# Optimization experiments

Measured on AMD Instinct MI355X. Metric: run time of the kernel, lower is better.

## Reference

```python
import jax, jax.numpy as jnp
import numpy as np

SIZE = 64
B, NMAX = 8, 24


def setup_inputs() -> dict:
    key = jax.random.key(0)
    ks = jax.random.split(key, 8)
    # valid boxes: top-left in [0,400), width/height in [10,210)
    xy = jax.random.uniform(ks[0], (B, NMAX, 2)) * 400.0
    wh = jax.random.uniform(ks[1], (B, NMAX, 2)) * 200.0 + 10.0
    bboxes = jnp.concatenate([xy, xy + wh], axis=-1)  # [B,N,4] (x1,y1,x2,y2)
    num_obj = jax.random.randint(ks[2], (B,), 2, NMAX + 1)
    conv1_w = jax.random.normal(ks[3], (64, 2, 5, 5)) * 0.1
    conv1_b = jnp.zeros((64,), jnp.float32)
    conv2_w = jax.random.normal(ks[4], (32, 64, 5, 5)) * 0.05
    conv2_b = jnp.zeros((32,), jnp.float32)
    lin_w = jax.random.normal(ks[5], (5408, 4800)) * 0.01
    lin_b = jnp.zeros((4800,), jnp.float32)
    return dict(bboxes=bboxes, num_obj=num_obj, conv1_w=conv1_w, conv1_b=conv1_b,
                conv2_w=conv2_w, conv2_b=conv2_b, lin_w=lin_w, lin_b=lin_b)


def _pair_indices(num_obj):
    # ragged pair construction on host; num_obj is an integer constant input
    n = np.asarray(num_obj)
    bs, is_, js = [], [], []
    for b in range(n.shape[0]):
        ii, jj = np.triu_indices(int(n[b]), k=1)
        bs.append(np.full(ii.shape, b, dtype=np.int32))
        is_.append(ii.astype(np.int32))
        js.append(jj.astype(np.int32))
    return np.concatenate(bs), np.concatenate(is_), np.concatenate(js)


def _get_sp(boxA, boxB):
    # DRG-style spatial map: rescale both boxes into the union-box frame
    # (aspect preserving, shorter axis centered), rasterize as binary masks.
    # boxA, boxB: [M,4] -> [M,2,64,64]
    u1 = jnp.minimum(boxA[:, 0], boxB[:, 0])
    v1 = jnp.minimum(boxA[:, 1], boxB[:, 1])
    u2 = jnp.maximum(boxA[:, 2], boxB[:, 2])
    v2 = jnp.maximum(boxA[:, 3], boxB[:, 3])
    w = u2 - u1
    h = v2 - v1
    scale = (SIZE - 1.0) / jnp.maximum(jnp.maximum(w, h), 1e-6)
    offx = jnp.where(h >= w, (SIZE - 1.0 - w * scale) * 0.5, 0.0)
    offy = jnp.where(w > h, (SIZE - 1.0 - h * scale) * 0.5, 0.0)

    xs = jnp.arange(SIZE, dtype=jnp.float32)[None, None, :]
    ys = jnp.arange(SIZE, dtype=jnp.float32)[None, :, None]

    def rast(box):
        x1 = jnp.round((box[:, 0] - u1) * scale + offx)[:, None, None]
        y1 = jnp.round((box[:, 1] - v1) * scale + offy)[:, None, None]
        x2 = jnp.round((box[:, 2] - u1) * scale + offx)[:, None, None]
        y2 = jnp.round((box[:, 3] - v1) * scale + offy)[:, None, None]
        m = (xs >= x1) & (xs <= x2) & (ys >= y1) & (ys <= y2)
        return m.astype(jnp.float32)

    return jnp.stack([rast(boxA), rast(boxB)], axis=1)


def _conv(x, w, b):
    y = jax.lax.conv_general_dilated(x, w, (1, 1), 'VALID',
                                     dimension_numbers=('NCHW', 'OIHW', 'NCHW'))
    return y + b[None, :, None, None]


def _pool(x):
    return jax.lax.reduce_window(x, -jnp.inf, jax.lax.max,
                                 (1, 1, 2, 2), (1, 1, 2, 2), 'VALID')


def reference(bboxes, num_obj, conv1_w, conv1_b, conv2_w, conv2_b, lin_w, lin_b):
    bi, ii, ji = _pair_indices(num_obj)
    boxA = bboxes[bi, ii]                       # [M,4]
    boxB = bboxes[bi, ji]                       # [M,4]
    sp = _get_sp(boxA, boxB)                    # [M,2,64,64]
    x = jax.nn.relu(_conv(sp, conv1_w, conv1_b))   # [M,64,60,60]
    x = _pool(x)                                   # [M,64,30,30]
    x = jax.nn.relu(_conv(x, conv2_w, conv2_b))    # [M,32,26,26]
    x = _pool(x)                                   # [M,32,13,13]
    x = x.reshape(x.shape[0], -1)                  # [M,5408]
    feat = jax.nn.relu(x @ lin_w + lin_b)          # [M,4800]
    slicing = jnp.stack([jnp.asarray(bi), jnp.asarray(ii), jnp.asarray(ji)],
                        axis=1).astype(jnp.float32)  # [M,3]
    return feat, slicing
```

## Files before the change

### kernel.cpp

```cpp
#include <hip/hip_runtime.h>
#include <hip/hip_bf16.h>

typedef __attribute__((ext_vector_type(8))) short short8;
typedef __attribute__((ext_vector_type(4))) float f32x4;

__device__ inline unsigned short f2bf(float x) {
  unsigned u = __float_as_uint(x);
  unsigned rounding = 0x7FFFu + ((u >> 16) & 1u);
  return (unsigned short)((u + rounding) >> 16);
}
__device__ inline float bf2f(unsigned short u) {
  return __uint_as_float(((unsigned)u) << 16);
}
__device__ inline void gload_lds16(const void* g, void* l) {
  __builtin_amdgcn_global_load_lds(
      (const __attribute__((address_space(1))) unsigned int*)g,
      (__attribute__((address_space(3))) unsigned int*)l, 16, 0, 0);
}

#define KPAD 5440
#define NPAD 4864
#define X1Q  32768

__global__ void prep_pairs(const float* __restrict__ bboxes,
                           const int* __restrict__ num_obj, int M,
                           int* __restrict__ pairTab,
                           float* __restrict__ slicing) {
  __shared__ int cum[9];
  if (threadIdx.x == 0) {
    int c = 0; cum[0] = 0;
    for (int b = 0; b < 8; b++) { int n = num_obj[b]; c += n*(n-1)/2; cum[b+1] = c; }
  }
  __syncthreads();
  for (int m = threadIdx.x; m < M; m += blockDim.x) {
    int b = 0;
    while (b < 7 && m >= cum[b+1]) b++;
    int p = m - cum[b];
    int n = num_obj[b];
    int i = 0, rem = p;
    while (rem >= (n - 1 - i)) { rem -= (n - 1 - i); i++; }
    int j = i + 1 + rem;
    const float* A = bboxes + (b*24 + i)*4;
    const float* Bb = bboxes + (b*24 + j)*4;
    float ax1=A[0], ay1=A[1], ax2=A[2], ay2=A[3];
    float bx1=Bb[0], by1=Bb[1], bx2=Bb[2], by2=Bb[3];
    float u1 = fminf(ax1,bx1), v1 = fminf(ay1,by1);
    float u2 = fmaxf(ax2,bx2), v2 = fmaxf(ay2,by2);
    float w = u2-u1, h = v2-v1;
    float scale = 63.0f / fmaxf(fmaxf(w,h), 1e-6f);
    float offx = (h >= w) ? __fmul_rn(63.0f - __fmul_rn(w,scale), 0.5f) : 0.0f;
    float offy = (w > h)  ? __fmul_rn(63.0f - __fmul_rn(h,scale), 0.5f) : 0.0f;
    int* t = pairTab + m*8;
    t[0] = (int)rintf(__fadd_rn(__fmul_rn(ax1-u1, scale), offx));
    t[1] = (int)rintf(__fadd_rn(__fmul_rn(ay1-v1, scale), offy));
    t[2] = (int)rintf(__fadd_rn(__fmul_rn(ax2-u1, scale), offx));
    t[3] = (int)rintf(__fadd_rn(__fmul_rn(ay2-v1, scale), offy));
    t[4] = (int)rintf(__fadd_rn(__fmul_rn(bx1-u1, scale), offx));
    t[5] = (int)rintf(__fadd_rn(__fmul_rn(by1-v1, scale), offy));
    t[6] = (int)rintf(__fadd_rn(__fmul_rn(bx2-u1, scale), offx));
    t[7] = (int)rintf(__fadd_rn(__fmul_rn(by2-v1, scale), offy));
    slicing[m*3+0] = (float)b;
    slicing[m*3+1] = (float)i;
    slicing[m*3+2] = (float)j;
  }
}

__global__ void prep_tables(const float* __restrict__ w1, const float* __restrict__ b1,
                            const float* __restrict__ w2,
                            float* __restrict__ T, unsigned short* __restrict__ W2B) {
  int idx = blockIdx.x*256 + threadIdx.x;
  if (idx < 86528) {
    int o = idx & 63;
    int t = idx >> 6;
    int rxi = t % 26; t /= 26;
    int ryi = t % 26;
    int c = t / 26;
    int ky0 = ryi/5, ky1 = ryi%5, kx0 = rxi/5, kx1 = rxi%5;
    float s = 0.f;
    for (int ky = ky0; ky <= ky1; ky++)
      for (int kx = kx0; kx <= kx1; kx++)
        s += w1[((o*2 + c)*5 + ky)*5 + kx];
    T[idx] = s + 0.5f * b1[o];
  } else if (idx < 86528 + 53248) {
    int i = idx - 86528;
    int j = i & 7;
    int ln = (i >> 3) & 63;
    int r1 = i >> 9;
    int mt = r1 & 1;
    int r2 = r1 >> 1;
    int s = r2 % 13;
    int pp = r2 / 13;
    int oc = mt*16 + (ln & 15);
    int q = ln >> 4;
    int kyx = 2*s + (q >> 1);
    int ic = pp*16 + ((q & 1) << 3) + j;
    float val = 0.f;
    if (kyx < 25) val = w2[((oc*64 + ic)*5 + kyx/5)*5 + (kyx%5)];
    W2B[i] = f2bf(val);
  }
}

__global__ __launch_bounds__(256) void prep_wt(const float* __restrict__ lw,
                                               unsigned short* __restrict__ Wt) {
  __shared__ unsigned short tile[64][65];
  int k0 = blockIdx.x*64, n0 = blockIdx.y*64;
  for (int i = threadIdx.x; i < 64*64; i += 256) {
    int r = i >> 6, cdx = i & 63;
    int k = k0 + r, n = n0 + cdx;
    float v = (k < 5408) ? lw[(size_t)k*4800 + n] : 0.f;
    tile[r][cdx] = f2bf(v);
  }
  __syncthreads();
  for (int i = threadIdx.x; i < 64*64; i += 256) {
    int r = i >> 6, cdx = i & 63;
    int n = n0 + r, k = k0 + cdx;
    Wt[(size_t)n*KPAD + k] = tile[cdx][r];
  }
}

__global__ __launch_bounds__(256) void conv1_pool(
    const int* __restrict__ pairTab, const float* __restrict__ T,
    unsigned short* __restrict__ X1) {
  __shared__ unsigned char rIdx[4][64];
  int blk = blockIdx.x;
  int m = blk >> 2, pp = blk & 3;
  int tid = threadIdx.x;
  const int* pt = pairTab + m*8;

  if (tid < 240) {
    int qq = tid % 60, which = tid / 60;
    int lo, hi;
    if (which == 0)      { lo = pt[1]; hi = pt[3]; }
    else if (which == 1) { lo = pt[5]; hi = pt[7]; }
    else if (which == 2) { lo = pt[0]; hi = pt[2]; }
    else                 { lo = pt[4]; hi = pt[6]; }
    int k0 = lo - qq; if (k0 < 0) k0 = 0;
    int k1 = hi - qq; if (k1 > 4) k1 = 4;
    rIdx[which][qq] = (k0 > k1) ? (unsigned char)25 : (unsigned char)(k0*5 + k1);
  }
  __syncthreads();

  char* X1q = (char*)X1 + (size_t)blk * X1Q;
  for (int item = tid; item < 1800; item += 256) {
    int pos = item >> 1;
    int icg = item & 1;
    int ch0 = pp*16 + icg*8;
    int py = pos / 30, px = pos % 30;
    float best[8];
#pragma unroll
    for (int j = 0; j < 8; j++) best[j] = -1e30f;
#pragma unroll
    for (int d = 0; d < 4; d++) {
      int y = py*2 + (d>>1), x = px*2 + (d&1);
      int rya = rIdx[0][y], ryb = rIdx[1][y];
      int rxa = rIdx[2][x], rxb = rIdx[3][x];
      const float* Ta = T + (((rya)*26 + rxa)<<6) + ch0;
      const float* Tb = T + (((26 + ryb)*26 + rxb)<<6) + ch0;
      f32x4 a0 = *(const f32x4*)Ta, a1 = *(const f32x4*)(Ta+4);
      f32x4 c0 = *(const f32x4*)Tb, c1 = *(const f32x4*)(Tb+4);
#pragma unroll
      for (int j = 0; j < 4; j++) {
        best[j]   = fmaxf(best[j],   a0[j]+c0[j]);
        best[4+j] = fmaxf(best[4+j], a1[j]+c1[j]);
      }
    }
    short8 v;
#pragma unroll
    for (int j = 0; j < 8; j++)
      v[j] = (short)f2bf(fmaxf(best[j], 0.f));
    int byte = pos*32 + ((icg ^ ((pos>>2)&1))<<4);
    *(short8*)(X1q + byte) = v;
  }
}

__global__ __launch_bounds__(512) void conv2_mfma(
    const unsigned short* __restrict__ X1, const unsigned short* __restrict__ W2B,
    const float* __restrict__ b2, unsigned short* __restrict__ X, int M) {
  __shared__ char smem[2*X1Q];
  int m = blockIdx.x;
  int tid = threadIdx.x, lane = tid & 63, wid = tid >> 6;
  const char* X1m = (const char*)X1 + (size_t)m*4*X1Q;

  int ntile = (wid < 4) ? 6 : 5;
  int tstart = (wid < 4) ? wid*6 : 24 + (wid-4)*5;
  int rowbase[6];
#pragma unroll
  for (int tt = 0; tt < 6; tt++) {
    int pos = (tstart + tt)*16 + (lane & 15);
    if (pos > 675) pos = 675;
    rowbase[tt] = (pos/26)*30 + (pos % 26);
  }
  f32x4 acc[6][2];
#pragma unroll
  for (int tt = 0; tt < 6; tt++) {
    acc[tt][0] = (f32x4){0.f,0.f,0.f,0.f};
    acc[tt][1] = (f32x4){0.f,0.f,0.f,0.f};
  }

  int q = lane >> 4;
  int qh = q >> 1;
  int qs = q & 1;

  auto stageq = [&](int buf, int qtr) {
    const char* src = X1m + (size_t)qtr * X1Q;
    char* dst = smem + buf * X1Q;
#pragma unroll
    for (int c = 0; c < 4; c++) {
      int chunk = wid + c*8;
      gload_lds16(src + chunk*1024 + lane*16, dst + chunk*1024);
    }
  };

  stageq(0, 0);
  __syncthreads();
  for (int pp = 0; pp < 4; pp++) {
    if (pp < 3) stageq((pp+1) & 1, pp+1);
    const char* pb = smem + (pp & 1) * X1Q;
    for (int s = 0; s < 13; s++) {
      const unsigned short* wptr = W2B + (size_t)(pp*13 + s)*1024 + lane*8;
      short8 a0 = *(const short8*)wptr;
      short8 a1 = *(const short8*)(wptr + 512);
      int kyx = 2*s + qh; if (kyx > 24) kyx = 24;
      int radd = (kyx/5)*30 + (kyx%5);
#pragma unroll
      for (int tt = 0; tt < 6; tt++) {
        if (tt < ntile) {
          int row = rowbase[tt] + radd;
          int byte = row*32 + ((qs ^ ((row>>2)&1))<<4);
          short8 bv = *(const short8*)(pb + byte);
          acc[tt][0] = __builtin_amdgcn_mfma_f32_16x16x32_bf16(a0, bv, acc[tt][0], 0, 0, 0);
          acc[tt][1] = __builtin_amdgcn_mfma_f32_16x16x32_bf16(a1, bv, acc[tt][1], 0, 0, 0);
        }
      }
    }
    __syncthreads();
  }
  unsigned short* p1 = (unsigned short*)smem;
#pragma unroll
  for (int tt = 0; tt < 6; tt++) {
    if (tt < ntile) {
      int pos = (tstart + tt)*16 + (lane & 15);
      if (pos <= 675) {
#pragma unroll
        for (int mt = 0; mt < 2; mt++)
#pragma unroll
          for (int r = 0; r < 4; r++) {
            int oc = mt*16 + q*4 + r;
            p1[oc*676 + pos] = f2bf(acc[tt][mt][r]);
          }
      }
    }
  }
  __syncthreads();
  for (int f = tid; f < 5408; f += 512) {
    int oc = f / 169, rem = f % 169;
    int py = rem / 13, px = rem % 13;
    const unsigned short* c2 = p1 + oc*676 + py*52 + px*2;
    float v = fmaxf(fmaxf(bf2f(c2[0]), bf2f(c2[1])), fmaxf(bf2f(c2[26]), bf2f(c2[27])));
    X[(size_t)m*KPAD + f] = f2bf(fmaxf(v + b2[oc], 0.f));
  }
  if (tid < 32) X[(size_t)m*KPAD + 5408 + tid] = 0;
}

__global__ __launch_bounds__(256) void gemm_lin(
    const unsigned short* __restrict__ X, const unsigned short* __restrict__ Wt,
    const float* __restrict__ lin_b, float* __restrict__ P, float* __restrict__ out,
    int M, int Mpad, int splits) {
  __shared__ unsigned short As[2][4096];
  __shared__ unsigned short Bs[2][8192];
  int tid = threadIdx.x, lane = tid & 63, wid = tid >> 6;
  int m0 = blockIdx.x * 64, n0 = blockIdx.y * 128;
  int ks = blockIdx.z;
  int itBeg = (ks * 85) / splits, itEnd = ((ks + 1) * 85) / splits;
  int wm = wid >> 1, wn = wid & 1;

  f32x4 acc[2][4];
#pragma unroll
  for (int i = 0; i < 2; i++)
#pragma unroll
    for (int j = 0; j < 4; j++) acc[i][j] = (f32x4){0.f,0.f,0.f,0.f};

  int rsub = lane >> 3;
  int kslot = (lane & 7) ^ rsub;
  int kg = lane >> 4;

  auto stage = [&](int buf, int it) {
    size_t kof = (size_t)it * 64 + kslot * 8;
#pragma unroll
    for (int cc = 0; cc < 2; cc++) {
      int chunk = wid + cc*4;
      int gm = m0 + chunk*8 + rsub;
      gload_lds16(X + (size_t)gm*KPAD + kof, (char*)As[buf] + chunk*1024);
    }
#pragma unroll
    for (int cc = 0; cc < 4; cc++) {
      int chunk = wid + cc*4;
      int gn = n0 + chunk*8 + rsub;
      gload_lds16(Wt + (size_t)gn*KPAD + kof, (char*)Bs[buf] + chunk*1024);
    }
  };

  stage(0, itBeg);
  __syncthreads();
  int cur = 0;
  for (int it = itBeg; it < itEnd; ++it) {
    if (it + 1 < itEnd) stage(cur ^ 1, it + 1);
#pragma unroll
    for (int ksub = 0; ksub < 2; ++ksub) {
      int slot = ksub*4 + kg;
      short8 af[2], bfr[4];
#pragma unroll
      for (int mf = 0; mf < 2; mf++) {
        int r = wm*32 + mf*16 + (lane & 15);
        af[mf] = *(const short8*)((const char*)As[cur] + r*128 + ((slot ^ (lane&7))<<4));
      }
#pragma unroll
      for (int nf = 0; nf < 4; nf++) {
        int r = wn*64 + nf*16 + (lane & 15);
        bfr[nf] = *(const short8*)((const char*)Bs[cur] + r*128 + ((slot ^ (lane&7))<<4));
      }
#pragma unroll
      for (int mf = 0; mf < 2; mf++)
#pragma unroll
        for (int nf = 0; nf < 4; nf++)
          acc[mf][nf] = __builtin_amdgcn_mfma_f32_16x16x32_bf16(af[mf], bfr[nf], acc[mf][nf], 0, 0, 0);
    }
    __syncthreads();
    cur ^= 1;
  }

  if (splits == 1) {
#pragma unroll
    for (int mf = 0; mf < 2; mf++)
#pragma unroll
      for (int nf = 0; nf < 4; nf++) {
        int n = n0 + wn*64 + nf*16 + (lane & 15);
#pragma unroll
        for (int r = 0; r < 4; r++) {
          int mm = m0 + wm*32 + mf*16 + ((lane>>4)<<2) + r;
          if (mm < M && n < 4800)
            out[(size_t)mm*4800 + n] = fmaxf(acc[mf][nf][r] + lin_b[n], 0.f);
        }
      }
  } else {
    float* Pp = P + (size_t)ks * Mpad * NPAD;
#pragma unroll
    for (int mf = 0; mf < 2; mf++)
#pragma unroll
      for (int nf = 0; nf < 4; nf++) {
        int n = n0 + wn*64 + nf*16 + (lane & 15);
#pragma unroll
        for (int r = 0; r < 4; r++) {
          int mm = m0 + wm*32 + mf*16 + ((lane>>4)<<2) + r;
          Pp[(size_t)mm*NPAD + n] = acc[mf][nf][r];
        }
      }
  }
}

__global__ void reduce_out(const float* __restrict__ P, const float* __restrict__ lb,
                           float* __restrict__ out, int M, int Mpad, int splits) {
  int total = M * 1200;
  for (int idx = blockIdx.x*256 + threadIdx.x; idx < total; idx += gridDim.x*256) {
    int m = idx / 1200, qq = idx - m*1200;
    int n = qq * 4;
    f32x4 s = *(const f32x4*)(P + (size_t)m*NPAD + n);
    for (int sidx = 1; sidx < splits; sidx++)
      s += *(const f32x4*)(P + (size_t)sidx*Mpad*NPAD + (size_t)m*NPAD + n);
    f32x4 b = *(const f32x4*)(lb + n);
    f32x4 r;
#pragma unroll
    for (int j = 0; j < 4; j++) r[j] = fmaxf(s[j] + b[j], 0.f);
    *(f32x4*)(out + (size_t)m*4800 + n) = r;
  }
}

extern "C" void kernel_launch(void* const* d_in, const int* in_sizes, int n_in,
                              void* d_out, int out_size, void* d_ws, size_t ws_size,
                              hipStream_t stream) {
  const float* bboxes = (const float*)d_in[0];
  const int*   num_obj = (const int*)d_in[1];
  const float* w1 = (const float*)d_in[2];
  const float* b1 = (const float*)d_in[3];
  const float* w2 = (const float*)d_in[4];
  const float* b2 = (const float*)d_in[5];
  const float* lw = (const float*)d_in[6];
  const float* lb = (const float*)d_in[7];
  float* out = (float*)d_out;
  int M = out_size / 4803;
  int Mpad = (M + 63) & ~63;

  auto align512 = [](size_t x) { return (x + 511) & ~(size_t)511; };
  size_t fixed = 0;
  fixed += align512((size_t)M*8*4);
  fixed += align512((size_t)86528*4);
  fixed += align512((size_t)53248*2);
  fixed += align512((size_t)4800*KPAD*2);
  fixed += align512((size_t)Mpad*KPAD*2);
  fixed += align512((size_t)M*4*X1Q);
  int splits = 4;
  while (splits > 1 && fixed + align512((size_t)splits*Mpad*NPAD*4) > ws_size) splits >>= 1;

  char* ws = (char*)d_ws;
  size_t off = 0;
  auto alloc = [&](size_t bytes) {
    off = align512(off);
    char* p = ws + off;
    off += bytes;
    return p;
  };
  int* pairTab = (int*)alloc((size_t)M*8*4);
  float* T = (float*)alloc((size_t)86528*4);
  unsigned short* W2B = (unsigned short*)alloc((size_t)53248*2);
  unsigned short* Wt = (unsigned short*)alloc((size_t)4800*KPAD*2);
  unsigned short* X = (unsigned short*)alloc((size_t)Mpad*KPAD*2);
  unsigned short* X1 = (unsigned short*)alloc((size_t)M*4*X1Q);
  float* P = (splits > 1) ? (float*)alloc((size_t)splits*Mpad*NPAD*4) : nullptr;

  prep_pairs<<<1, 256, 0, stream>>>(bboxes, num_obj, M, pairTab, out + (size_t)M*4800);
  prep_tables<<<(86528+53248+255)/256, 256, 0, stream>>>(w1, b1, w2, T, W2B);
  prep_wt<<<dim3(85, 75), 256, 0, stream>>>(lw, Wt);
  conv1_pool<<<M*4, 256, 0, stream>>>(pairTab, T, X1);
  conv2_mfma<<<M, 512, 0, stream>>>(X1, W2B, b2, X, M);
  gemm_lin<<<dim3(Mpad/64, 38, splits), 256, 0, stream>>>(X, Wt, lb, P, out, M, Mpad, splits);
  if (splits > 1)
    reduce_out<<<1024, 256, 0, stream>>>(P, lb, out, M, Mpad, splits);
}
```

Baseline: 346.5 us.

## Split conv2 per pair into two row-halves with smaller blocks and LDS

The conv2 MFMA kernel now launches two 256-thread blocks per pair instead of one 512-thread block. Each block computes half of the output rows: rows 0-13 for the first block and rows 14-25 for the second. It stages only the input rows that half needs, into a smaller double-buffered LDS region. The goal is more blocks, less LDS per block and higher occupancy, so more pairs' conv2 work can overlap. The cost is some redundant input loading across the halo rows and more per-wave tiles per block.

```diff
diff --git a/kernel.cpp b/kernel.cpp
--- a/kernel.cpp
+++ b/kernel.cpp
@@ -21,6 +21,7 @@
 #define KPAD 5440
 #define NPAD 4864
 #define X1Q  32768
+#define SBUF 17408
 
 __global__ void prep_pairs(const float* __restrict__ bboxes,
                            const int* __restrict__ num_obj, int M,
@@ -173,22 +174,32 @@
   }
 }
 
-__global__ __launch_bounds__(512) void conv2_mfma(
+__global__ __launch_bounds__(256) void conv2_mfma(
     const unsigned short* __restrict__ X1, const unsigned short* __restrict__ W2B,
     const float* __restrict__ b2, unsigned short* __restrict__ X, int M) {
-  __shared__ char smem[2*X1Q];
-  int m = blockIdx.x;
+  __shared__ char smem[2*SBUF];
+  int blk = blockIdx.x;
+  int m = blk >> 1, h = blk & 1;
   int tid = threadIdx.x, lane = tid & 63, wid = tid >> 6;
   const char* X1m = (const char*)X1 + (size_t)m*4*X1Q;
 
-  int ntile = (wid < 4) ? 6 : 5;
-  int tstart = (wid < 4) ? wid*6 : 24 + (wid-4)*5;
+  int oy0    = h ? 14 : 0;
+  int npos   = h ? 312 : 364;
+  int ntiles = h ? 20 : 23;
+  int row0   = h ? 416 : 0;
+  int ncall  = h ? 16 : 17;
+
+  int tbase = ntiles >> 2, trem = ntiles & 3;
+  int ntile  = tbase + (wid < trem ? 1 : 0);
+  int tstart = (wid < trem) ? wid*(tbase+1) : trem*(tbase+1) + (wid-trem)*tbase;
+
   int rowbase[6];
 #pragma unroll
   for (int tt = 0; tt < 6; tt++) {
     int pos = (tstart + tt)*16 + (lane & 15);
-    if (pos > 675) pos = 675;
-    rowbase[tt] = (pos/26)*30 + (pos % 26);
+    if (pos > npos-1) pos = npos-1;
+    int oy = oy0 + pos/26;
+    rowbase[tt] = oy*30 + pos%26;
   }
   f32x4 acc[6][2];
 #pragma unroll
@@ -197,17 +208,16 @@
     acc[tt][1] = (f32x4){0.f,0.f,0.f,0.f};
   }
 
-  int q = lane >> 4;
-  int qh = q >> 1;
-  int qs = q & 1;
+  int q = lane >> 4, qh = q >> 1, qs = q & 1;
 
   auto stageq = [&](int buf, int qtr) {
-    const char* src = X1m + (size_t)qtr * X1Q;
-    char* dst = smem + buf * X1Q;
-#pragma unroll
-    for (int c = 0; c < 4; c++) {
-      int chunk = wid + c*8;
-      gload_lds16(src + chunk*1024 + lane*16, dst + chunk*1024);
+    const char* src = X1m + (size_t)qtr * X1Q + row0*32;
+    char* dst = smem + buf * SBUF;
+#pragma unroll
+    for (int c = 0; c < 5; c++) {
+      int chunk = wid + c*4;
+      if (chunk < ncall)
+        gload_lds16(src + chunk*1024 + lane*16, dst + chunk*1024);
     }
   };
 
@@ -215,7 +225,7 @@
   __syncthreads();
   for (int pp = 0; pp < 4; pp++) {
     if (pp < 3) stageq((pp+1) & 1, pp+1);
-    const char* pb = smem + (pp & 1) * X1Q;
+    const char* pb = smem + (pp & 1) * SBUF;
     for (int s = 0; s < 13; s++) {
       const unsigned short* wptr = W2B + (size_t)(pp*13 + s)*1024 + lane*8;
       short8 a0 = *(const short8*)wptr;
@@ -226,7 +236,7 @@
       for (int tt = 0; tt < 6; tt++) {
         if (tt < ntile) {
           int row = rowbase[tt] + radd;
-          int byte = row*32 + ((qs ^ ((row>>2)&1))<<4);
+          int byte = (row - row0)*32 + ((qs ^ ((row>>2)&1))<<4);
           short8 bv = *(const short8*)(pb + byte);
           acc[tt][0] = __builtin_amdgcn_mfma_f32_16x16x32_bf16(a0, bv, acc[tt][0], 0, 0, 0);
           acc[tt][1] = __builtin_amdgcn_mfma_f32_16x16x32_bf16(a1, bv, acc[tt][1], 0, 0, 0);
@@ -240,26 +250,30 @@
   for (int tt = 0; tt < 6; tt++) {
     if (tt < ntile) {
       int pos = (tstart + tt)*16 + (lane & 15);
-      if (pos <= 675) {
+      if (pos < npos) {
 #pragma unroll
         for (int mt = 0; mt < 2; mt++)
 #pragma unroll
           for (int r = 0; r < 4; r++) {
             int oc = mt*16 + q*4 + r;
-            p1[oc*676 + pos] = f2bf(acc[tt][mt][r]);
+            p1[oc*npos + pos] = f2bf(acc[tt][mt][r]);
           }
       }
     }
   }
   __syncthreads();
-  for (int f = tid; f < 5408; f += 512) {
-    int oc = f / 169, rem = f % 169;
-    int py = rem / 13, px = rem % 13;
-    const unsigned short* c2 = p1 + oc*676 + py*52 + px*2;
+  int nout = h ? 6 : 7;
+  int oypb = h ? 7 : 0;
+  for (int f = tid; f < 32*nout*13; f += 256) {
+    int ocl = f / (nout*13), rem2 = f % (nout*13);
+    int oyl = rem2 / 13, px = rem2 % 13;
+    int oyp = oypb + oyl;
+    int posl = (oyp*2 - oy0)*26 + px*2;
+    const unsigned short* c2 = p1 + ocl*npos + posl;
     float v = fmaxf(fmaxf(bf2f(c2[0]), bf2f(c2[1])), fmaxf(bf2f(c2[26]), bf2f(c2[27])));
-    X[(size_t)m*KPAD + f] = f2bf(fmaxf(v + b2[oc], 0.f));
-  }
-  if (tid < 32) X[(size_t)m*KPAD + 5408 + tid] = 0;
+    X[(size_t)m*KPAD + ocl*169 + oyp*13 + px] = f2bf(fmaxf(v + b2[ocl], 0.f));
+  }
+  if (h == 0 && tid < 32) X[(size_t)m*KPAD + 5408 + tid] = 0;
 }
 
 __global__ __launch_bounds__(256) void gemm_lin(
@@ -421,7 +435,7 @@
   prep_tables<<<(86528+53248+255)/256, 256, 0, stream>>>(w1, b1, w2, T, W2B);
   prep_wt<<<dim3(85, 75), 256, 0, stream>>>(lw, Wt);
   conv1_pool<<<M*4, 256, 0, stream>>>(pairTab, T, X1);
-  conv2_mfma<<<M, 512, 0, stream>>>(X1, W2B, b2, X, M);
+  conv2_mfma<<<M*2, 256, 0, stream>>>(X1, W2B, b2, X, M);
   gemm_lin<<<dim3(Mpad/64, 38, splits), 256, 0, stream>>>(X, Wt, lb, P, out, M, Mpad, splits);
   if (splits > 1)
     reduce_out<<<1024, 256, 0, stream>>>(P, lb, out, M, Mpad, splits);
```

After: 403.1 us. 16.3% more time.
